# Performance work log

Hardware: AMD Instinct MI355X
Metric: run time of the kernel (lower is better)

Reference implementation:

```python
import jax, jax.numpy as jnp
import numpy as np

DIM = 1024
NUM_HEADS = 16
HEAD_DIM = DIM // NUM_HEADS
B, NQ, NKV = 8, 1024, 1024


def setup_inputs() -> dict:
    key = jax.random.key(0)
    ks = jax.random.split(key, 6)
    std = 1.0 / np.sqrt(DIM)
    return {
        "x": jax.random.normal(ks[0], (B, NQ, DIM), dtype=jnp.float32),
        "context": jax.random.normal(ks[1], (B, NKV, DIM), dtype=jnp.float32),
        "Wq": jax.random.normal(ks[2], (DIM, DIM), dtype=jnp.float32) * std,
        "bq": jnp.zeros((DIM,), dtype=jnp.float32),
        "Wk": jax.random.normal(ks[3], (DIM, DIM), dtype=jnp.float32) * std,
        "bk": jnp.zeros((DIM,), dtype=jnp.float32),
        "Wv": jax.random.normal(ks[4], (DIM, DIM), dtype=jnp.float32) * std,
        "bv": jnp.zeros((DIM,), dtype=jnp.float32),
        "Wo": jax.random.normal(ks[5], (DIM, DIM), dtype=jnp.float32) * std,
        "bo": jnp.zeros((DIM,), dtype=jnp.float32),
    }


def _split_heads(t):
    # [B, N, D] -> [B, H, N, Hd]
    b, n, _ = t.shape
    return t.reshape(b, n, NUM_HEADS, HEAD_DIM).transpose(0, 2, 1, 3)


def reference(x, context, Wq, bq, Wk, bk, Wv, bv, Wo, bo):
    scale = HEAD_DIM ** -0.5
    q = _split_heads(x @ Wq + bq)        # [B,H,Nq,Hd]
    k = _split_heads(context @ Wk + bk)  # [B,H,Nk,Hd]
    v = _split_heads(context @ Wv + bv)  # [B,H,Nk,Hd]
    # scaled dot-product attention
    scores = jnp.einsum("bhqd,bhkd->bhqk", q, k) * scale
    attn = jax.nn.softmax(scores, axis=-1)
    out = jnp.einsum("bhqk,bhkd->bhqd", attn, v)  # [B,H,Nq,Hd]
    out = out.transpose(0, 2, 1, 3).reshape(x.shape[0], x.shape[1], DIM)
    return out @ Wo + bo
```

## Files before the change

kernel.cpp:

```cpp
#include <hip/hip_runtime.h>
#include <stdint.h>

using bf16x8 = __attribute__((ext_vector_type(8))) short;
using f32x4  = __attribute__((ext_vector_type(4))) float;
using f32x2  = __attribute__((ext_vector_type(2))) float;
using u16    = unsigned short;
using u16x4  = __attribute__((ext_vector_type(4))) unsigned short;
using u16x8  = __attribute__((ext_vector_type(8))) unsigned short;
using bf16x2v = __attribute__((ext_vector_type(2))) __bf16;

#define LOG2E 1.4426950408889634f

#if __has_builtin(__builtin_amdgcn_exp2f)
#define fast_exp2(x) __builtin_amdgcn_exp2f(x)
#else
#define fast_exp2(x) exp2f(x)
#endif

static __device__ __forceinline__ u16 bf16r(float f) {
  union { __bf16 h; u16 u; } v; v.h = (__bf16)f; return v.u;
}
static __device__ __forceinline__ unsigned pk2(float a, float b) {
  union { bf16x2v h; unsigned u; } r;
  r.h = __builtin_convertvector((f32x2){a, b}, bf16x2v);
  return r.u;
}
static __device__ __forceinline__ u16x4 pk4(float a, float b, float c, float d) {
  union { unsigned u[2]; u16x4 v; } r;
  r.u[0] = pk2(a, b); r.u[1] = pk2(c, d);
  return r.v;
}

static __device__ __forceinline__ void async_ld16(u16* lds, const u16* g) {
  __builtin_amdgcn_global_load_lds(
      (const __attribute__((address_space(1))) void*)g,
      (__attribute__((address_space(3))) void*)lds,
      16, 0, 0);
}

static __device__ __forceinline__ f32x4 mfma16(bf16x8 a, bf16x8 b, f32x4 c) {
  return __builtin_amdgcn_mfma_f32_16x16x32_bf16(a, b, c, 0, 0, 0);
}

__global__ void prep_kernel(const float* __restrict__ x, const float* __restrict__ ctx,
                            const float* __restrict__ W0, const float* __restrict__ W1,
                            const float* __restrict__ W2, const float* __restrict__ W3,
                            u16* __restrict__ Xb, u16* __restrict__ Cb,
                            u16* __restrict__ T0, u16* __restrict__ T1,
                            u16* __restrict__ T2, u16* __restrict__ T3) {
  int bid = blockIdx.x;
  int t = threadIdx.x;
  if (bid < 4096) {
    const int n4 = 2097152;
    int i = bid * 256 + t;
    const int stride = 4096 * 256;
#pragma unroll
    for (int it = 0; it < 4; ++it, i += stride) {
      const float4* src = (i < n4) ? ((const float4*)x + i) : ((const float4*)ctx + (i - n4));
      u16x4* dst = (i < n4) ? ((u16x4*)Xb + i) : ((u16x4*)Cb + (i - n4));
      float4 v = *src;
      *dst = pk4(v.x, v.y, v.z, v.w);
    }
    return;
  }
  int b2 = bid - 4096;
  int z = b2 >> 8, rem = b2 & 255;
  const float* W = (z == 0) ? W0 : (z == 1) ? W1 : (z == 2) ? W2 : W3;
  u16* T = (z == 0) ? T0 : (z == 1) ? T1 : (z == 2) ? T2 : T3;
  __shared__ float tile[64][65];
  int k0 = (rem & 15) * 64, n0 = (rem >> 4) * 64;
#pragma unroll
  for (int i = 0; i < 4; ++i) {
    int kl = i * 16 + (t >> 4); int nl = (t & 15) * 4;
    float4 v = *(const float4*)(W + (size_t)(k0 + kl) * 1024 + n0 + nl);
    tile[kl][nl] = v.x; tile[kl][nl + 1] = v.y; tile[kl][nl + 2] = v.z; tile[kl][nl + 3] = v.w;
  }
  __syncthreads();
#pragma unroll
  for (int i = 0; i < 16; ++i) {
    int idx = i * 256 + t; int nl = idx >> 6; int kl = idx & 63;
    T[(size_t)(n0 + nl) * 1024 + k0 + kl] = bf16r(tile[kl][nl]);
  }
}

__global__ __launch_bounds__(256, 2) void proj_gemm_kernel(
    const u16* __restrict__ Xb, const u16* __restrict__ Cb,
    const u16* __restrict__ Wqt, const u16* __restrict__ Wkt, const u16* __restrict__ Wvt,
    const float* __restrict__ bq, const float* __restrict__ bk, const float* __restrict__ bv,
    u16* __restrict__ Qo, u16* __restrict__ Ko, u16* __restrict__ Vo) {
  __shared__ u16 smem[32768];
  u16* sA = smem;
  u16* sB = smem + 16384;
  int z = blockIdx.z;
  const u16* A    = (z == 0) ? Xb : Cb;
  const u16* Bt   = (z == 0) ? Wqt : (z == 1) ? Wkt : Wvt;
  const float* bias = (z == 0) ? bq : (z == 1) ? bk : bv;
  int m0 = blockIdx.x * 128, n0 = blockIdx.y * 128;
  int t = threadIdx.x, w = t >> 6, lane = t & 63, quad = lane >> 4, lc = lane & 15;
  int wm = (w & 1) * 64, wn = (w >> 1) * 64;
  int sx = lc & 7;

  f32x4 acc[4][4];
  f32x4 z4 = {0.f, 0.f, 0.f, 0.f};
#pragma unroll
  for (int i = 0; i < 4; ++i)
#pragma unroll
    for (int j = 0; j < 4; ++j) acc[i][j] = z4;

  const u16* Abase = A  + (size_t)m0 * 1024;
  const u16* Bbase = Bt + (size_t)n0 * 1024;

  auto STAGE = [&](int s, int kt) {
#pragma unroll
    for (int i = 0; i < 4; ++i) {
      int c = i * 256 + t; int row = c >> 3; int cc = c & 7;
      async_ld16(sA + s * 8192 + c * 8,
                 Abase + (size_t)row * 1024 + kt * 64 + ((cc ^ (row & 7)) * 8));
    }
#pragma unroll
    for (int i = 0; i < 4; ++i) {
      int c = i * 256 + t; int row = c >> 3; int cc = c & 7;
      async_ld16(sB + s * 8192 + c * 8,
                 Bbase + (size_t)row * 1024 + kt * 64 + ((cc ^ (row & 7)) * 8));
    }
  };

  STAGE(0, 0);
  STAGE(1, 1);

  for (int kt = 0; kt < 16; ++kt) {
    int s = kt & 1;
    if (kt < 15) asm volatile("s_waitcnt vmcnt(8)" ::: "memory");
    else         asm volatile("s_waitcnt vmcnt(0)" ::: "memory");
    __builtin_amdgcn_s_barrier();
    const u16* pA = sA + s * 8192;
    const u16* pB = sB + s * 8192;
#pragma unroll
    for (int ks = 0; ks < 2; ++ks) {
      bf16x8 af[4], bfr[4];
#pragma unroll
      for (int i = 0; i < 4; ++i)
        af[i]  = *(const bf16x8*)(pA + (wm + i * 16 + lc) * 64 + (((ks * 4 + quad) ^ sx)) * 8);
#pragma unroll
      for (int i = 0; i < 4; ++i)
        bfr[i] = *(const bf16x8*)(pB + (wn + i * 16 + lc) * 64 + (((ks * 4 + quad) ^ sx)) * 8);
      __builtin_amdgcn_s_setprio(1);
#pragma unroll
      for (int qi = 0; qi < 4; ++qi)
#pragma unroll
        for (int nj = 0; nj < 4; ++nj) acc[qi][nj] = mfma16(af[qi], bfr[nj], acc[qi][nj]);
      __builtin_amdgcn_s_setprio(0);
    }
    __builtin_amdgcn_s_barrier();
    if (kt < 14) STAGE(s, kt + 2);
  }

  if (z < 2) {
    u16* dst = (z == 0) ? Qo : Ko;
    float scl = (z == 0) ? 0.125f * LOG2E : 1.0f;
#pragma unroll
    for (int qi = 0; qi < 4; ++qi)
#pragma unroll
      for (int nj = 0; nj < 4; ++nj) {
        int n = n0 + wn + nj * 16 + lc;
        float bvv = bias[n];
        int hh = n >> 6, d = n & 63;
#pragma unroll
        for (int r = 0; r < 4; ++r) {
          int m = m0 + wm + qi * 16 + quad * 4 + r;
          int bb = m >> 10, pos = m & 1023;
          float v = (acc[qi][nj][r] + bvv) * scl;
          dst[((size_t)(bb * 16 + hh) * 1024 + pos) * 64 + d] = bf16r(v);
        }
      }
  } else {
    __syncthreads();
    u16* Tw = smem + w * (64 * 66);
    int hh = (n0 + wn) >> 6;
    int mb = m0 + wm; int bb = mb >> 10; int pos0 = mb & 1023;
#pragma unroll
    for (int qi = 0; qi < 4; ++qi)
#pragma unroll
      for (int nj = 0; nj < 4; ++nj) {
        int lcc = nj * 16 + lc;
        float bvv = bias[n0 + wn + lcc];
#pragma unroll
        for (int r = 0; r < 4; ++r) {
          int lr = qi * 16 + quad * 4 + r;
          Tw[lr * 66 + lcc] = bf16r(acc[qi][nj][r] + bvv);
        }
      }
#pragma unroll
    for (int i = 0; i < 8; ++i) {
      int dl = i * 8 + (lane >> 3); int kv0 = (lane & 7) * 8;
      u16x8 pk;
#pragma unroll
      for (int j = 0; j < 8; ++j) pk[j] = Tw[(kv0 + j) * 66 + dl];
      *(u16x8*)(Vo + ((size_t)(bb * 16 + hh) * 64 + dl) * 1024 + pos0 + kv0) = pk;
    }
  }
}

__global__ __launch_bounds__(256, 4) void attn_kernel(const u16* __restrict__ Qb,
                                                      const u16* __restrict__ Kb,
                                                      const u16* __restrict__ Vt,
                                                      u16* __restrict__ Ab) {
  __shared__ u16 smem[16384];
  u16* sK = smem;
  u16* sV = smem + 4096;
  u16* sP = smem + 8192;
  int bid = blockIdx.x;
  int bh = (bid & 7) | ((bid >> 6) << 3);
  int qt = (bid >> 3) & 7;
  int bb = bh >> 4, hh = bh & 15;
  int t = threadIdx.x, w = t >> 6, lane = t & 63, quad = lane >> 4, lc = lane & 15;

  const u16* Qg = Qb + ((size_t)bh * 1024 + qt * 128 + w * 32) * 64;
  bf16x8 qf[2][2];
#pragma unroll
  for (int qi = 0; qi < 2; ++qi)
#pragma unroll
    for (int ks = 0; ks < 2; ++ks)
      qf[qi][ks] = *(const bf16x8*)(Qg + (qi * 16 + lc) * 64 + ks * 32 + quad * 8);

  f32x4 O[4][2];
  f32x4 z4 = {0.f, 0.f, 0.f, 0.f};
#pragma unroll
  for (int dj = 0; dj < 4; ++dj) { O[dj][0] = z4; O[dj][1] = z4; }
  float l_lane[2] = {0.f, 0.f};

  const u16* Kg = Kb + (size_t)bh * 65536;
  const u16* Vg = Vt + (size_t)bh * 65536;
  int r0 = t >> 3, gs = t & 7;

  auto STAGE_K = [&](int kt) {
#pragma unroll
    for (int i = 0; i < 2; ++i) {
      int r = r0 + i * 32;
      async_ld16(sK + i * 2048 + t * 8, Kg + (size_t)(kt * 64 + r) * 64 + (gs ^ (r & 7)) * 8);
    }
  };
  auto STAGE_V = [&](int kt) {
#pragma unroll
    for (int i = 0; i < 2; ++i) {
      int d = r0 + i * 32;
      async_ld16(sV + i * 2048 + t * 8, Vg + (size_t)d * 1024 + kt * 64 + (gs ^ (d & 7)) * 8);
    }
  };

  STAGE_K(0);
  STAGE_V(0);

  for (int kt = 0; kt < 16; ++kt) {
    asm volatile("s_waitcnt vmcnt(2)" ::: "memory");
    __builtin_amdgcn_s_barrier();

    f32x4 s[4][2];
#pragma unroll
    for (int kj = 0; kj < 4; ++kj) { s[kj][0] = z4; s[kj][1] = z4; }
    __builtin_amdgcn_s_setprio(1);
#pragma unroll
    for (int kj = 0; kj < 4; ++kj) {
      int kv = kj * 16 + lc;
#pragma unroll
      for (int ks = 0; ks < 2; ++ks) {
        bf16x8 a = *(const bf16x8*)(sK + kv * 64 + ((ks * 4 + quad) ^ (kv & 7)) * 8);
        s[kj][0] = mfma16(a, qf[0][ks], s[kj][0]);
        s[kj][1] = mfma16(a, qf[1][ks], s[kj][1]);
      }
    }
    __builtin_amdgcn_s_setprio(0);

#pragma unroll
    for (int qi = 0; qi < 2; ++qi) {
      int q = w * 32 + qi * 16 + lc;
#pragma unroll
      for (int kj = 0; kj < 4; ++kj) {
        float p0 = fast_exp2(s[kj][qi][0]);
        float p1 = fast_exp2(s[kj][qi][1]);
        float p2 = fast_exp2(s[kj][qi][2]);
        float p3 = fast_exp2(s[kj][qi][3]);
        l_lane[qi] += (p0 + p1) + (p2 + p3);
        int g = kj * 2 + (quad >> 1);
        *(u16x4*)(sP + q * 64 + ((g ^ (q & 7)) * 8) + (quad & 1) * 4) = pk4(p0, p1, p2, p3);
      }
    }

    asm volatile("s_waitcnt vmcnt(0)" ::: "memory");
    __builtin_amdgcn_s_barrier();
    if (kt < 15) STAGE_K(kt + 1);

    __builtin_amdgcn_s_setprio(1);
#pragma unroll
    for (int ks = 0; ks < 2; ++ks) {
      bf16x8 pb[2];
#pragma unroll
      for (int qi = 0; qi < 2; ++qi) {
        int q = w * 32 + qi * 16 + lc;
        pb[qi] = *(const bf16x8*)(sP + q * 64 + (((ks * 4 + quad) ^ (q & 7))) * 8);
      }
#pragma unroll
      for (int dj = 0; dj < 4; ++dj) {
        int d = dj * 16 + lc;
        bf16x8 va = *(const bf16x8*)(sV + d * 64 + (((ks * 4 + quad) ^ (d & 7))) * 8);
        O[dj][0] = mfma16(va, pb[0], O[dj][0]);
        O[dj][1] = mfma16(va, pb[1], O[dj][1]);
      }
    }
    __builtin_amdgcn_s_setprio(0);

    __builtin_amdgcn_s_barrier();
    if (kt < 15) STAGE_V(kt + 1);
  }

  float inv[2];
#pragma unroll
  for (int qi = 0; qi < 2; ++qi) {
    float l = l_lane[qi];
    l += __shfl_xor(l, 16);
    l += __shfl_xor(l, 32);
    inv[qi] = 1.f / l;
  }

  __syncthreads();
  u16* myP = smem + w * 2304;
#pragma unroll
  for (int qi = 0; qi < 2; ++qi)
#pragma unroll
    for (int dj = 0; dj < 4; ++dj)
      *(u16x4*)(myP + (qi * 16 + lc) * 72 + dj * 16 + quad * 4) =
          pk4(O[dj][qi][0] * inv[qi], O[dj][qi][1] * inv[qi],
              O[dj][qi][2] * inv[qi], O[dj][qi][3] * inv[qi]);
#pragma unroll
  for (int i = 0; i < 4; ++i) {
    int idx = i * 64 + lane; int ql = idx >> 3; int dg = idx & 7;
    u16x8 pk = *(const u16x8*)(myP + ql * 72 + dg * 8);
    *(u16x8*)(Ab + ((size_t)bb * 1024 + qt * 128 + w * 32 + ql) * 1024 + hh * 64 + dg * 8) = pk;
  }
}

__global__ __launch_bounds__(256, 2) void out_gemm_kernel(const u16* __restrict__ A,
                                                          const u16* __restrict__ Bt,
                                                          const float* __restrict__ bo,
                                                          float* __restrict__ out) {
  __shared__ u16 smem[32768];
  u16* sA = smem;
  u16* sB = smem + 16384;
  int m0 = blockIdx.x * 128, n0 = blockIdx.y * 128;
  int t = threadIdx.x, w = t >> 6, lane = t & 63, quad = lane >> 4, lc = lane & 15;
  int wm = (w & 1) * 64, wn = (w >> 1) * 64;
  int sx = lc & 7;
  f32x4 acc[4][4];
  f32x4 z4 = {0.f, 0.f, 0.f, 0.f};
#pragma unroll
  for (int i = 0; i < 4; ++i)
#pragma unroll
    for (int j = 0; j < 4; ++j) acc[i][j] = z4;

  const u16* Abase = A  + (size_t)m0 * 1024;
  const u16* Bbase = Bt + (size_t)n0 * 1024;

  auto STAGE = [&](int s, int kt) {
#pragma unroll
    for (int i = 0; i < 4; ++i) {
      int c = i * 256 + t; int row = c >> 3; int cc = c & 7;
      async_ld16(sA + s * 8192 + c * 8,
                 Abase + (size_t)row * 1024 + kt * 64 + ((cc ^ (row & 7)) * 8));
    }
#pragma unroll
    for (int i = 0; i < 4; ++i) {
      int c = i * 256 + t; int row = c >> 3; int cc = c & 7;
      async_ld16(sB + s * 8192 + c * 8,
                 Bbase + (size_t)row * 1024 + kt * 64 + ((cc ^ (row & 7)) * 8));
    }
  };

  STAGE(0, 0);
  STAGE(1, 1);

  for (int kt = 0; kt < 16; ++kt) {
    int s = kt & 1;
    if (kt < 15) asm volatile("s_waitcnt vmcnt(8)" ::: "memory");
    else         asm volatile("s_waitcnt vmcnt(0)" ::: "memory");
    __builtin_amdgcn_s_barrier();
    const u16* pA = sA + s * 8192;
    const u16* pB = sB + s * 8192;
#pragma unroll
    for (int ks = 0; ks < 2; ++ks) {
      bf16x8 af[4], bfr[4];
#pragma unroll
      for (int i = 0; i < 4; ++i)
        af[i]  = *(const bf16x8*)(pA + (wm + i * 16 + lc) * 64 + (((ks * 4 + quad) ^ sx)) * 8);
#pragma unroll
      for (int i = 0; i < 4; ++i)
        bfr[i] = *(const bf16x8*)(pB + (wn + i * 16 + lc) * 64 + (((ks * 4 + quad) ^ sx)) * 8);
      __builtin_amdgcn_s_setprio(1);
#pragma unroll
      for (int qi = 0; qi < 4; ++qi)
#pragma unroll
        for (int nj = 0; nj < 4; ++nj) acc[qi][nj] = mfma16(af[qi], bfr[nj], acc[qi][nj]);
      __builtin_amdgcn_s_setprio(0);
    }
    __builtin_amdgcn_s_barrier();
    if (kt < 14) STAGE(s, kt + 2);
  }

#pragma unroll
  for (int qi = 0; qi < 4; ++qi)
#pragma unroll
    for (int nj = 0; nj < 4; ++nj) {
      int n = n0 + wn + nj * 16 + lc;
      float bvv = bo[n];
#pragma unroll
      for (int r = 0; r < 4; ++r) {
        int m = m0 + wm + qi * 16 + quad * 4 + r;
        out[(size_t)m * 1024 + n] = acc[qi][nj][r] + bvv;
      }
    }
}

extern "C" void kernel_launch(void* const* d_in, const int* in_sizes, int n_in,
                              void* d_out, int out_size, void* d_ws, size_t ws_size,
                              hipStream_t stream) {
  const float* x   = (const float*)d_in[0];
  const float* ctx = (const float*)d_in[1];
  const float* Wq  = (const float*)d_in[2];
  const float* bq  = (const float*)d_in[3];
  const float* Wk  = (const float*)d_in[4];
  const float* bk  = (const float*)d_in[5];
  const float* Wv  = (const float*)d_in[6];
  const float* bv  = (const float*)d_in[7];
  const float* Wo  = (const float*)d_in[8];
  const float* bo  = (const float*)d_in[9];
  float* out = (float*)d_out;

  const size_t NE = (size_t)8192 * 1024;
  char* p = (char*)d_ws;
  u16* Xb  = (u16*)p;             p += NE * 2;
  u16* Cb  = (u16*)p;             p += NE * 2;
  u16* Wqt = (u16*)p;             p += (size_t)1024 * 1024 * 2;
  u16* Wkt = (u16*)p;             p += (size_t)1024 * 1024 * 2;
  u16* Wvt = (u16*)p;             p += (size_t)1024 * 1024 * 2;
  u16* Wot = (u16*)p;             p += (size_t)1024 * 1024 * 2;
  u16* Qb  = (u16*)p;             p += NE * 2;
  u16* Kb  = (u16*)p;             p += NE * 2;
  u16* Vtb = (u16*)p;             p += NE * 2;
  u16* Ab  = Xb;

  prep_kernel<<<5120, 256, 0, stream>>>(x, ctx, Wq, Wk, Wv, Wo,
                                        Xb, Cb, Wqt, Wkt, Wvt, Wot);
  proj_gemm_kernel<<<dim3(64, 8, 3), 256, 0, stream>>>(Xb, Cb, Wqt, Wkt, Wvt,
                                                       bq, bk, bv, Qb, Kb, Vtb);
  attn_kernel<<<1024, 256, 0, stream>>>(Qb, Kb, Vtb, Ab);
  out_gemm_kernel<<<dim3(64, 8), 256, 0, stream>>>(Ab, Wot, bo, out);
}
```

Baseline: 251.8 us.

## Fuse fp32-to-bf16 activation conversion into projection GEMM A-tile loading

Removes the separate conversion pass that wrote bf16 copies of x and context. The projection GEMM now loads fp32 A rows into registers one k-tile ahead, packs them to bf16 and writes them to swizzled LDS, while B still uses async global-to-LDS loads. This removes an intermediate write and read of the activations, but the GEMM reads twice the bytes per A tile and the A prefetch is register-staged, with an extra lgkmcnt wait.

Result: slower. 297.6 us (+18.2%).

```diff
diff --git a/kernel.cpp b/kernel.cpp
--- a/kernel.cpp
+++ b/kernel.cpp
@@ -42,29 +42,13 @@
   return __builtin_amdgcn_mfma_f32_16x16x32_bf16(a, b, c, 0, 0, 0);
 }
 
-__global__ void prep_kernel(const float* __restrict__ x, const float* __restrict__ ctx,
-                            const float* __restrict__ W0, const float* __restrict__ W1,
+__global__ void prep_kernel(const float* __restrict__ W0, const float* __restrict__ W1,
                             const float* __restrict__ W2, const float* __restrict__ W3,
-                            u16* __restrict__ Xb, u16* __restrict__ Cb,
                             u16* __restrict__ T0, u16* __restrict__ T1,
                             u16* __restrict__ T2, u16* __restrict__ T3) {
   int bid = blockIdx.x;
   int t = threadIdx.x;
-  if (bid < 4096) {
-    const int n4 = 2097152;
-    int i = bid * 256 + t;
-    const int stride = 4096 * 256;
-#pragma unroll
-    for (int it = 0; it < 4; ++it, i += stride) {
-      const float4* src = (i < n4) ? ((const float4*)x + i) : ((const float4*)ctx + (i - n4));
-      u16x4* dst = (i < n4) ? ((u16x4*)Xb + i) : ((u16x4*)Cb + (i - n4));
-      float4 v = *src;
-      *dst = pk4(v.x, v.y, v.z, v.w);
-    }
-    return;
-  }
-  int b2 = bid - 4096;
-  int z = b2 >> 8, rem = b2 & 255;
+  int z = bid >> 8, rem = bid & 255;
   const float* W = (z == 0) ? W0 : (z == 1) ? W1 : (z == 2) ? W2 : W3;
   u16* T = (z == 0) ? T0 : (z == 1) ? T1 : (z == 2) ? T2 : T3;
   __shared__ float tile[64][65];
@@ -84,7 +68,7 @@
 }
 
 __global__ __launch_bounds__(256, 2) void proj_gemm_kernel(
-    const u16* __restrict__ Xb, const u16* __restrict__ Cb,
+    const float* __restrict__ Xf, const float* __restrict__ Cf,
     const u16* __restrict__ Wqt, const u16* __restrict__ Wkt, const u16* __restrict__ Wvt,
     const float* __restrict__ bq, const float* __restrict__ bk, const float* __restrict__ bv,
     u16* __restrict__ Qo, u16* __restrict__ Ko, u16* __restrict__ Vo) {
@@ -92,7 +76,7 @@
   u16* sA = smem;
   u16* sB = smem + 16384;
   int z = blockIdx.z;
-  const u16* A    = (z == 0) ? Xb : Cb;
+  const float* Af = (z == 0) ? Xf : Cf;
   const u16* Bt   = (z == 0) ? Wqt : (z == 1) ? Wkt : Wvt;
   const float* bias = (z == 0) ? bq : (z == 1) ? bk : bv;
   int m0 = blockIdx.x * 128, n0 = blockIdx.y * 128;
@@ -107,16 +91,13 @@
 #pragma unroll
     for (int j = 0; j < 4; ++j) acc[i][j] = z4;
 
-  const u16* Abase = A  + (size_t)m0 * 1024;
+  int arow = t >> 1, ahalf = t & 1;
+  const float* Asrc = Af + (size_t)(m0 + arow) * 1024 + ahalf * 32;
+  u16* adst_row = sA + arow * 64;
+  int ar7 = arow & 7;
+
   const u16* Bbase = Bt + (size_t)n0 * 1024;
-
-  auto STAGE = [&](int s, int kt) {
-#pragma unroll
-    for (int i = 0; i < 4; ++i) {
-      int c = i * 256 + t; int row = c >> 3; int cc = c & 7;
-      async_ld16(sA + s * 8192 + c * 8,
-                 Abase + (size_t)row * 1024 + kt * 64 + ((cc ^ (row & 7)) * 8));
-    }
+  auto STAGE_B = [&](int s, int kt) {
 #pragma unroll
     for (int i = 0; i < 4; ++i) {
       int c = i * 256 + t; int row = c >> 3; int cc = c & 7;
@@ -125,13 +106,34 @@
     }
   };
 
-  STAGE(0, 0);
-  STAGE(1, 1);
+  float4 areg[8];
+#pragma unroll
+  for (int i = 0; i < 8; ++i) areg[i] = *(const float4*)(Asrc + i * 4);
+  asm volatile("" ::: "memory");
+  STAGE_B(0, 0);
+  asm volatile("" ::: "memory");
+  STAGE_B(1, 1);
 
   for (int kt = 0; kt < 16; ++kt) {
     int s = kt & 1;
-    if (kt < 15) asm volatile("s_waitcnt vmcnt(8)" ::: "memory");
+    if (kt < 15) asm volatile("s_waitcnt vmcnt(4)" ::: "memory");
     else         asm volatile("s_waitcnt vmcnt(0)" ::: "memory");
+#pragma unroll
+    for (int j = 0; j < 4; ++j) {
+      union { unsigned u[4]; u16x8 v; } pk;
+      pk.u[0] = pk2(areg[2 * j].x, areg[2 * j].y);
+      pk.u[1] = pk2(areg[2 * j].z, areg[2 * j].w);
+      pk.u[2] = pk2(areg[2 * j + 1].x, areg[2 * j + 1].y);
+      pk.u[3] = pk2(areg[2 * j + 1].z, areg[2 * j + 1].w);
+      int g = ahalf * 4 + j;
+      *(u16x8*)(adst_row + s * 8192 + ((g ^ ar7) * 8)) = pk.v;
+    }
+    if (kt < 15) {
+      const float* an = Asrc + (kt + 1) * 64;
+#pragma unroll
+      for (int i = 0; i < 8; ++i) areg[i] = *(const float4*)(an + i * 4);
+    }
+    asm volatile("s_waitcnt lgkmcnt(0)" ::: "memory");
     __builtin_amdgcn_s_barrier();
     const u16* pA = sA + s * 8192;
     const u16* pB = sB + s * 8192;
@@ -152,7 +154,7 @@
       __builtin_amdgcn_s_setprio(0);
     }
     __builtin_amdgcn_s_barrier();
-    if (kt < 14) STAGE(s, kt + 2);
+    if (kt < 14) STAGE_B(s, kt + 2);
   }
 
   if (z < 2) {
@@ -436,8 +438,7 @@
 
   const size_t NE = (size_t)8192 * 1024;
   char* p = (char*)d_ws;
-  u16* Xb  = (u16*)p;             p += NE * 2;
-  u16* Cb  = (u16*)p;             p += NE * 2;
+  u16* Ab  = (u16*)p;             p += NE * 2;
   u16* Wqt = (u16*)p;             p += (size_t)1024 * 1024 * 2;
   u16* Wkt = (u16*)p;             p += (size_t)1024 * 1024 * 2;
   u16* Wvt = (u16*)p;             p += (size_t)1024 * 1024 * 2;
@@ -445,11 +446,9 @@
   u16* Qb  = (u16*)p;             p += NE * 2;
   u16* Kb  = (u16*)p;             p += NE * 2;
   u16* Vtb = (u16*)p;             p += NE * 2;
-  u16* Ab  = Xb;
-
-  prep_kernel<<<5120, 256, 0, stream>>>(x, ctx, Wq, Wk, Wv, Wo,
-                                        Xb, Cb, Wqt, Wkt, Wvt, Wot);
-  proj_gemm_kernel<<<dim3(64, 8, 3), 256, 0, stream>>>(Xb, Cb, Wqt, Wkt, Wvt,
+
+  prep_kernel<<<1024, 256, 0, stream>>>(Wq, Wk, Wv, Wo, Wqt, Wkt, Wvt, Wot);
+  proj_gemm_kernel<<<dim3(64, 8, 3), 256, 0, stream>>>(x, ctx, Wqt, Wkt, Wvt,
                                                        bq, bk, bv, Qb, Kb, Vtb);
   attn_kernel<<<1024, 256, 0, stream>>>(Qb, Kb, Vtb, Ab);
   out_gemm_kernel<<<dim3(64, 8), 256, 0, stream>>>(Ab, Wot, bo, out);
```
